# Kernel tuning notes

Measured on AMD Instinct MI355X. Metric: run time of the kernel, lower is better.

## Reference

```python
import jax, jax.numpy as jnp
import numpy as np

B, N, E, F, G = 32, 512, 4, 128, 64
EMB, HID = 128, 256  # NodeEmbedding: Linear(E*G=256 -> 256) + BN + ELU + Linear(256 -> 128)
NUM_EDGES = 8192
BN_EPS = 1e-5


def setup_inputs() -> dict:
    key = jax.random.key(0)
    ks = jax.random.split(key, 8)
    X = jax.random.normal(ks[0], (B, N, F), dtype=jnp.float32)
    edges = jax.random.randint(ks[1], (B, E, 2, NUM_EDGES), 0, N, dtype=jnp.int64)
    # per-edge-type projection W_e: [F, G] (glorot)
    Ws = jax.random.normal(ks[2], (E, F, G), dtype=jnp.float32) * np.sqrt(2.0 / (F + G))
    # attention vectors a_e: [2G, 1]
    a = jax.random.normal(ks[3], (E, 2 * G, 1), dtype=jnp.float32) * (1.414 * np.sqrt(2.0 / (2 * G + 1)))
    lin0_w = jax.random.normal(ks[4], (E * G, HID), dtype=jnp.float32) * np.sqrt(2.0 / (E * G + HID))
    lin0_b = jnp.zeros((HID,), dtype=jnp.float32)
    bn_gamma = jnp.ones((HID,), dtype=jnp.float32)
    bn_beta = jnp.zeros((HID,), dtype=jnp.float32)
    lin1_w = jax.random.normal(ks[5], (HID, EMB), dtype=jnp.float32) * np.sqrt(2.0 / (HID + EMB))
    lin1_b = jnp.zeros((EMB,), dtype=jnp.float32)
    return {"X": X, "edges": edges, "Ws": Ws, "a": a, "lin0_w": lin0_w,
            "lin0_b": lin0_b, "bn_gamma": bn_gamma, "bn_beta": bn_beta,
            "lin1_w": lin1_w, "lin1_b": lin1_b}


def _dense_adj(edges):
    # COO -> dense, summing duplicates like torch.sparse_coo_tensor(...).to_dense()
    b_ix = jnp.arange(B)[:, None, None]
    e_ix = jnp.arange(E)[None, :, None]
    src = edges[:, :, 0, :]
    dst = edges[:, :, 1, :]
    A = jnp.zeros((B, E, N, N), dtype=jnp.float32)
    return A.at[b_ix, e_ix, src, dst].add(1.0)


def reference(X, edges, Ws, a, lin0_w, lin0_b, bn_gamma, bn_beta, lin1_w, lin1_b):
    A = _dense_adj(edges)                                   # [B,E,N,N]
    Wh = jnp.einsum('bnf,efg->beng', X, Ws)                 # [B,E,N,G]
    Wh1 = jnp.einsum('beng,ego->beno', Wh, a[:, :G, :])     # [B,E,N,1]
    Wh2 = jnp.einsum('beng,ego->beno', Wh, a[:, G:, :])     # [B,E,N,1]
    scores = (Wh1 + jnp.swapaxes(Wh2, 2, 3)) * A            # [B,E,N,N] (masked-to-0, NOT -inf: faithful)
    att = jax.nn.softmax(scores, axis=-1)
    H = jnp.einsum('benm,bemg->beng', att * A, Wh)          # [B,E,N,G]
    H = jnp.transpose(H, (0, 2, 1, 3)).reshape(B * N, E * G)
    # NodeEmbedding MLP (BatchNorm1d in training mode: batch stats, biased var)
    h = H @ lin0_w + lin0_b
    mu = jnp.mean(h, axis=0)
    var = jnp.mean((h - mu) ** 2, axis=0)
    h = (h - mu) * jax.lax.rsqrt(var + BN_EPS) * bn_gamma + bn_beta
    h = jax.nn.elu(h)
    out = h @ lin1_w + lin1_b
    return out.reshape(B, N, EMB)
```

## Files before the change

### kernel.cpp

```cpp
#include <hip/hip_runtime.h>

#define Bx 32
#define Nx 512
#define Ex 4
#define Fx 128
#define Gx 64
#define HIDx 256
#define EMBx 128
#define NEDGE 8192

typedef __attribute__((ext_vector_type(8))) short bf16x8;
typedef __attribute__((ext_vector_type(4))) float f32x4;

#define L2E 1.44269504f

__device__ __forceinline__ ushort f2bf(float x) {
    unsigned int u = __float_as_uint(x);
    u += 0x7fffu + ((u >> 16) & 1u);
    return (ushort)(u >> 16);
}
__device__ __forceinline__ float bf2f(ushort h) {
    return __uint_as_float(((unsigned int)h) << 16);
}

__global__ __launch_bounds__(512) void k0b(const int* __restrict__ edges,
                                           const float* __restrict__ w0,
                                           const float* __restrict__ w1f,
                                           const float* __restrict__ Wsf,
                                           ushort* __restrict__ W0T,
                                           ushort* __restrict__ W1T,
                                           ushort* __restrict__ WsT,
                                           ushort* __restrict__ binned,
                                           int* __restrict__ offs) {
    __shared__ int hist8[8][8];
    __shared__ int offl[9];
    __shared__ int cur[8];
    int blk = blockIdx.x, tid = threadIdx.x;
    if (blk < 128) {
        int wave = tid >> 6;
        if (tid < 64) ((int*)hist8)[tid] = 0;
        __syncthreads();
        const int4* s4p = (const int4*)(edges + (size_t)blk * 2 * NEDGE);
        const int4* d4p = (const int4*)(edges + (size_t)blk * 2 * NEDGE + NEDGE);
        for (int i = tid; i < NEDGE / 4; i += 512) {
            int4 s4 = s4p[i];
            atomicAdd(&hist8[wave][s4.x >> 6], 1);
            atomicAdd(&hist8[wave][s4.y >> 6], 1);
            atomicAdd(&hist8[wave][s4.z >> 6], 1);
            atomicAdd(&hist8[wave][s4.w >> 6], 1);
        }
        __syncthreads();
        if (tid == 0) {
            int run = 0;
            for (int t = 0; t < 8; ++t) {
                offl[t] = run;
                int s = 0;
                #pragma unroll
                for (int w = 0; w < 8; ++w) s += hist8[w][t];
                run += s;
            }
            offl[8] = run;
            for (int t = 0; t <= 8; ++t) offs[blk * 9 + t] = offl[t];
        }
        __syncthreads();
        if (tid < 8) cur[tid] = offl[tid];
        __syncthreads();
        ushort* bout = binned + (size_t)blk * NEDGE;
        for (int i = tid; i < NEDGE / 4; i += 512) {
            int4 s4 = s4p[i]; int4 d4 = d4p[i];
            int ss[4] = {s4.x, s4.y, s4.z, s4.w};
            int dd[4] = {d4.x, d4.y, d4.z, d4.w};
            #pragma unroll
            for (int u = 0; u < 4; ++u) {
                int t = ss[u] >> 6;
                int pos = atomicAdd(&cur[t], 1);
                bout[pos] = (ushort)(((ss[u] & 63) << 9) | dd[u]);
            }
        }
    } else if (blk < 256) {
        int idx = (blk - 128) * 512 + tid;
        int j = idx >> 8, k = idx & 255;
        W0T[j * HIDx + k] = f2bf(w0[k * HIDx + j]);
    } else if (blk < 320) {
        int idx = (blk - 256) * 512 + tid;
        int j = idx >> 8, k = idx & 255;
        W1T[j * HIDx + k] = f2bf(w1f[k * EMBx + j]);
    } else {
        int idx = (blk - 320) * 512 + tid;
        int eg = idx >> 7, f = idx & 127;
        WsT[eg * Fx + f] = f2bf(Wsf[((eg >> 6) * Fx + f) * Gx + (eg & 63)]);
    }
}

__global__ __launch_bounds__(256) void k1_wh(const float* __restrict__ X,
                                             const ushort* __restrict__ WsT,
                                             const float* __restrict__ a,
                                             ushort* __restrict__ Whb,
                                             float* __restrict__ w1,
                                             float* __restrict__ w2) {
    __shared__ ushort sXb[64 * 128];
    int id = blockIdx.x;
    int e = id & 3;
    int rest = id >> 2;
    int tile = rest & 7;
    int b = rest >> 3;
    int be = b * 4 + e;
    int n0 = tile * 64;
    int tid = threadIdx.x;
    for (int i = tid; i < 2048; i += 256) {
        int row = i >> 5, kq = i & 31;
        float4 xv = *(const float4*)&X[(size_t)(b * Nx + n0 + row) * Fx + kq * 4];
        ushort4 hv;
        hv.x = f2bf(xv.x); hv.y = f2bf(xv.y); hv.z = f2bf(xv.z); hv.w = f2bf(xv.w);
        unsigned int byteo = ((unsigned int)(row * 256 + kq * 8)) ^ (((unsigned int)(row & 7)) << 4);
        *(ushort4*)((char*)sXb + byteo) = hv;
    }
    __syncthreads();
    int wave = tid >> 6, lane = tid & 63;
    int arow = lane & 15, kg = lane >> 4;
    int row = wave * 16 + arow;
    f32x4 acc[4];
    #pragma unroll
    for (int t = 0; t < 4; ++t) acc[t] = (f32x4){0.f, 0.f, 0.f, 0.f};
    const ushort* WT = WsT + e * Gx * Fx;
    unsigned int aswz = ((unsigned int)(row & 7)) << 4;
    #pragma unroll
    for (int ks = 0; ks < 4; ++ks) {
        unsigned int abyte = ((unsigned int)(row * 256 + ks * 64 + kg * 16)) ^ aswz;
        bf16x8 af = *(const bf16x8*)((const char*)sXb + abyte);
        #pragma unroll
        for (int jt = 0; jt < 4; ++jt) {
            bf16x8 bf = *(const bf16x8*)&WT[(size_t)(jt * 16 + arow) * Fx + ks * 32 + kg * 8];
            acc[jt] = __builtin_amdgcn_mfma_f32_16x16x32_bf16(af, bf, acc[jt], 0, 0, 0);
        }
    }
    float a1v[4], a2v[4];
    #pragma unroll
    for (int jt = 0; jt < 4; ++jt) {
        a1v[jt] = a[e * 2 * Gx + jt * 16 + arow];
        a2v[jt] = a[e * 2 * Gx + Gx + jt * 16 + arow];
    }
    int m0 = n0 + wave * 16 + kg * 4;
    #pragma unroll
    for (int jt = 0; jt < 4; ++jt) {
        int g = jt * 16 + arow;
        ushort4 v;
        v.x = f2bf(acc[jt][0]); v.y = f2bf(acc[jt][1]);
        v.z = f2bf(acc[jt][2]); v.w = f2bf(acc[jt][3]);
        *(ushort4*)&Whb[((size_t)be * Gx + g) * Nx + m0] = v;
    }
    #pragma unroll
    for (int reg = 0; reg < 4; ++reg) {
        float p1 = acc[0][reg] * a1v[0] + acc[1][reg] * a1v[1] + acc[2][reg] * a1v[2] + acc[3][reg] * a1v[3];
        float p2 = acc[0][reg] * a2v[0] + acc[1][reg] * a2v[1] + acc[2][reg] * a2v[2] + acc[3][reg] * a2v[3];
        #pragma unroll
        for (int off = 1; off < 16; off <<= 1) {
            p1 += __shfl_xor(p1, off, 64);
            p2 += __shfl_xor(p2, off, 64);
        }
        if (arow == 0) {
            w1[be * Nx + m0 + reg] = p1;
            w2[be * Nx + m0 + reg] = p2;
        }
    }
}

__global__ __launch_bounds__(512) void k2_att(const ushort* __restrict__ binned,
                                              const int* __restrict__ offs,
                                              const ushort* __restrict__ Whb,
                                              const float* __restrict__ w1g,
                                              const float* __restrict__ w2g,
                                              ushort* __restrict__ Hb) {
    __shared__ ushort P[64 * 512];
    __shared__ float sw2[512];
    __shared__ float sw1[64];
    __shared__ float sinv[64];
    __shared__ float rowsum[64];
    __shared__ ushort olist[4096];
    __shared__ int ocnt;
    unsigned int* cnt = (unsigned int*)P;
    int be = blockIdx.x; int b = be >> 2; int e = be & 3;
    int tile = blockIdx.y; int n0 = tile * 64;
    int tid = threadIdx.x;
    for (int i = tid; i < 64 * 132; i += 512) cnt[i] = 0u;
    {
        uint4 z = {0u, 0u, 0u, 0u};
        uint4* pu = (uint4*)((char*)P + 33792);
        for (int i = tid; i < 1984; i += 512) pu[i] = z;
    }
    sw2[tid] = w2g[be * Nx + tid] * L2E;
    if (tid < 64) {
        sw1[tid] = w1g[be * Nx + n0 + tid] * L2E;
        rowsum[tid] = 512.f;
    }
    if (tid == 0) ocnt = 0;
    __syncthreads();
    int t0 = offs[be * 9 + tile], t1 = offs[be * 9 + tile + 1];
    const ushort* bin = binned + (size_t)be * NEDGE;
    int lane = tid & 63;
    for (int i = t0 + tid; i < t1; i += 512) {
        unsigned int pk = bin[i];
        unsigned int sh = (pk & 3u) * 8;
        unsigned int old = atomicAdd(&cnt[(pk >> 9) * 132 + ((pk & 511u) >> 2)], 1u << sh);
        bool own = ((old >> sh) & 255u) == 0u;
        unsigned long long m = __ballot(own);
        if (m) {
            int leader = __ffsll((long long)m) - 1;
            int base = 0;
            if (lane == leader) base = atomicAdd(&ocnt, __popcll(m));
            base = __shfl(base, leader, 64);
            if (own) {
                int ix = base + __popcll(m & ((1ull << lane) - 1ull));
                if (ix < 4096) olist[ix] = (ushort)pk;
            }
        }
    }
    __syncthreads();
    int tot = ocnt; if (tot > 4096) tot = 4096;
    const unsigned char* cb = (const unsigned char*)cnt;
    ushort pbv[8]; int pkv[8];
    #pragma unroll
    for (int u = 0; u < 8; ++u) {
        int i = tid + u * 512;
        int pk = -1; ushort pb = 0;
        if (i < tot) {
            pk = (int)olist[i];
            int r = pk >> 9, d = pk & 511;
            float c = (float)cb[r * 528 + d];
            float ew = __builtin_exp2f(fminf((sw1[r] + sw2[d]) * c, 120.f));
            atomicAdd(&rowsum[r], ew - 1.f);
            pb = f2bf(ew * c);
        }
        pkv[u] = pk; pbv[u] = pb;
    }
    __syncthreads();
    {
        uint4 z = {0u, 0u, 0u, 0u};
        uint4* pu = (uint4*)P;
        for (int i = tid; i < 2112; i += 512) pu[i] = z;
    }
    __syncthreads();
    #pragma unroll
    for (int u = 0; u < 8; ++u) {
        if (pkv[u] >= 0) {
            int r = pkv[u] >> 9, d = pkv[u] & 511;
            unsigned int byteo = ((unsigned int)(r * 1024 + d * 2)) ^ (((unsigned int)(r & 7)) << 4);
            *(ushort*)((char*)P + byteo) = pbv[u];
        }
    }
    if (tid < 64) sinv[tid] = 1.f / rowsum[tid];
    int wave = tid >> 6;
    int wr2 = wave >> 2, wc = wave & 3;
    int rowa = wr2 * 32 + (lane & 15);
    int rowb = rowa + 16;
    int kgrp = lane >> 4;
    const ushort* WB = Whb + (size_t)be * Gx * Nx;
    int g0 = wc * 16 + (lane & 15);
    const ushort* Bp = WB + (size_t)g0 * Nx + kgrp * 8;
    bf16x8 bpre0 = *(const bf16x8*)(Bp + 0 * 32);
    bf16x8 bpre1 = *(const bf16x8*)(Bp + 1 * 32);
    bf16x8 bpre2 = *(const bf16x8*)(Bp + 2 * 32);
    bf16x8 bpre3 = *(const bf16x8*)(Bp + 3 * 32);
    __syncthreads();
    f32x4 acca = {0.f, 0.f, 0.f, 0.f};
    f32x4 accb = {0.f, 0.f, 0.f, 0.f};
    unsigned int aswza = ((unsigned int)(rowa & 7)) << 4;
    __builtin_amdgcn_s_setprio(1);
    #pragma unroll
    for (int ks = 0; ks < 16; ++ks) {
        bf16x8 bfv;
        if (ks == 0) bfv = bpre0;
        else if (ks == 1) bfv = bpre1;
        else if (ks == 2) bfv = bpre2;
        else if (ks == 3) bfv = bpre3;
        else bfv = *(const bf16x8*)(Bp + ks * 32);
        unsigned int ka = (unsigned int)(ks * 64 + kgrp * 16);
        unsigned int offa = ((unsigned int)(rowa * 1024) + ka) ^ aswza;
        unsigned int offb = ((unsigned int)(rowb * 1024) + ka) ^ aswza;
        bf16x8 afa = *(const bf16x8*)((const char*)P + offa);
        bf16x8 afb = *(const bf16x8*)((const char*)P + offb);
        acca = __builtin_amdgcn_mfma_f32_16x16x32_bf16(afa, bfv, acca, 0, 0, 0);
        accb = __builtin_amdgcn_mfma_f32_16x16x32_bf16(afb, bfv, accb, 0, 0, 0);
    }
    __builtin_amdgcn_s_setprio(0);
    #pragma unroll
    for (int reg = 0; reg < 4; ++reg) {
        int ra = n0 + wr2 * 32 + kgrp * 4 + reg;
        float iva = sinv[wr2 * 32 + kgrp * 4 + reg];
        float ivb = sinv[wr2 * 32 + 16 + kgrp * 4 + reg];
        Hb[((size_t)(b * Nx) + ra) * (Ex * Gx) + e * Gx + wc * 16 + (lane & 15)] =
            f2bf(acca[reg] * iva);
        Hb[((size_t)(b * Nx) + ra + 16) * (Ex * Gx) + e * Gx + wc * 16 + (lane & 15)] =
            f2bf(accb[reg] * ivb);
    }
}

__global__ __launch_bounds__(256) void k3_lin0(const ushort* __restrict__ Hb,
                                               const ushort* __restrict__ W0T,
                                               const float* __restrict__ lin0_b,
                                               ushort* __restrict__ h_pre,
                                               float* __restrict__ partials) {
    __shared__ float red_s[2][256], red_q[2][256];
    int tid = threadIdx.x, wave = tid >> 6, lane = tid & 63;
    int wr = wave >> 1, wc = wave & 1;
    int row0 = blockIdx.x * 32 + wr * 16;
    int arow = lane & 15, kg = lane >> 4;
    const ushort* A = Hb + (size_t)(row0 + arow) * HIDx;
    f32x4 acc[8];
    #pragma unroll
    for (int t = 0; t < 8; ++t) acc[t] = (f32x4){0.f, 0.f, 0.f, 0.f};
    #pragma unroll
    for (int ks = 0; ks < 8; ++ks) {
        int k0 = ks * 32 + kg * 8;
        bf16x8 af = *(const bf16x8*)&A[k0];
        #pragma unroll
        for (int jt = 0; jt < 8; ++jt) {
            bf16x8 bf = *(const bf16x8*)&W0T[(size_t)(wc * 128 + jt * 16 + arow) * HIDx + k0];
            acc[jt] = __builtin_amdgcn_mfma_f32_16x16x32_bf16(af, bf, acc[jt], 0, 0, 0);
        }
    }
    #pragma unroll
    for (int jt = 0; jt < 8; ++jt) {
        int col = wc * 128 + jt * 16 + arow;
        float b = lin0_b[col];
        float s = 0.f, q = 0.f;
        #pragma unroll
        for (int reg = 0; reg < 4; ++reg) {
            float v = acc[jt][reg] + b;
            h_pre[(size_t)(row0 + kg * 4 + reg) * HIDx + col] = f2bf(v);
            s += v; q += v * v;
        }
        s += __shfl_xor(s, 16, 64); s += __shfl_xor(s, 32, 64);
        q += __shfl_xor(q, 16, 64); q += __shfl_xor(q, 32, 64);
        if (lane < 16) { red_s[wr][col] = s; red_q[wr][col] = q; }
    }
    __syncthreads();
    int j = tid;
    partials[(size_t)blockIdx.x * 2 * HIDx + j] = red_s[0][j] + red_s[1][j];
    partials[(size_t)blockIdx.x * 2 * HIDx + HIDx + j] = red_q[0][j] + red_q[1][j];
}

__global__ __launch_bounds__(256) void k3b_stats(const float* __restrict__ partials,
                                                 const float* __restrict__ gamma,
                                                 const float* __restrict__ beta,
                                                 float* __restrict__ sb) {
    __shared__ float rs[8][32], rq[8][32];
    int jl = threadIdx.x & 31, sl = threadIdx.x >> 5;
    int j = blockIdx.x * 32 + jl;
    float s = 0.f, q = 0.f;
    for (int blk = sl; blk < 512; blk += 8) {
        s += partials[blk * 512 + j];
        q += partials[blk * 512 + 256 + j];
    }
    rs[sl][jl] = s; rq[sl][jl] = q;
    __syncthreads();
    if (threadIdx.x < 32) {
        float S = 0.f, Q = 0.f;
        #pragma unroll
        for (int t = 0; t < 8; ++t) { S += rs[t][jl]; Q += rq[t][jl]; }
        const float invM = 1.f / 16384.f;
        float mu = S * invM;
        float var = fmaxf(Q * invM - mu * mu, 0.f);
        float sc = gamma[j] * rsqrtf(var + 1e-5f);
        sb[j] = sc;
        sb[256 + j] = beta[j] - mu * sc;
    }
}

__global__ __launch_bounds__(256) void k4_lin1(const ushort* __restrict__ h_pre,
                                               const float* __restrict__ sb,
                                               const ushort* __restrict__ W1T,
                                               const float* __restrict__ lin1_b,
                                               float* __restrict__ out) {
    int tid = threadIdx.x, wave = tid >> 6, lane = tid & 63;
    int wr = wave >> 1, wc = wave & 1;
    int row0 = blockIdx.x * 32 + wr * 16;
    int arow = lane & 15, kg = lane >> 4;
    const ushort* A = h_pre + (size_t)(row0 + arow) * HIDx;
    f32x4 acc[4];
    #pragma unroll
    for (int t = 0; t < 4; ++t) acc[t] = (f32x4){0.f, 0.f, 0.f, 0.f};
    #pragma unroll
    for (int ks = 0; ks < 8; ++ks) {
        int k0 = ks * 32 + kg * 8;
        bf16x8 hv = *(const bf16x8*)&A[k0];
        float4 sc0 = *(const float4*)&sb[k0];
        float4 sc1 = *(const float4*)&sb[k0 + 4];
        float4 bi0 = *(const float4*)&sb[256 + k0];
        float4 bi1 = *(const float4*)&sb[256 + k0 + 4];
        float scv[8] = {sc0.x, sc0.y, sc0.z, sc0.w, sc1.x, sc1.y, sc1.z, sc1.w};
        float biv[8] = {bi0.x, bi0.y, bi0.z, bi0.w, bi1.x, bi1.y, bi1.z, bi1.w};
        bf16x8 af;
        #pragma unroll
        for (int u = 0; u < 8; ++u) {
            float v = bf2f((ushort)hv[u]) * scv[u] + biv[u];
            v = v > 0.f ? v : expm1f(v);
            af[u] = (short)f2bf(v);
        }
        #pragma unroll
        for (int jt = 0; jt < 4; ++jt) {
            bf16x8 bf = *(const bf16x8*)&W1T[(size_t)(wc * 64 + jt * 16 + arow) * HIDx + k0];
            acc[jt] = __builtin_amdgcn_mfma_f32_16x16x32_bf16(af, bf, acc[jt], 0, 0, 0);
        }
    }
    #pragma unroll
    for (int jt = 0; jt < 4; ++jt) {
        int col = wc * 64 + jt * 16 + arow;
        float b = lin1_b[col];
        #pragma unroll
        for (int reg = 0; reg < 4; ++reg)
            out[(size_t)(row0 + kg * 4 + reg) * EMBx + col] = acc[jt][reg] + b;
    }
}

extern "C" void kernel_launch(void* const* d_in, const int* in_sizes, int n_in,
                              void* d_out, int out_size, void* d_ws, size_t ws_size,
                              hipStream_t stream) {
    const float* X      = (const float*)d_in[0];
    const int*   edges  = (const int*)d_in[1];
    const float* Ws     = (const float*)d_in[2];
    const float* a      = (const float*)d_in[3];
    const float* lin0_w = (const float*)d_in[4];
    const float* lin0_b = (const float*)d_in[5];
    const float* gamma  = (const float*)d_in[6];
    const float* beta   = (const float*)d_in[7];
    const float* lin1_w = (const float*)d_in[8];
    const float* lin1_b = (const float*)d_in[9];
    float* ws = (float*)d_ws;

    ushort* Whb     = (ushort*)ws;
    ushort* h_pre   = (ushort*)ws;
    ushort* binned  = (ushort*)ws + 4194304;
    int*    offs    = (int*)(ws + 2621440);
    ushort* Hb      = (ushort*)(ws + 4194304);
    float*  w1      = ws + 8388608;
    float*  w2      = ws + 8454144;
    float*  partials= ws + 8519680;
    float*  sb      = ws + 8781824;
    ushort* WsT     = (ushort*)(ws + 8782336);
    ushort* W0T     = (ushort*)(ws + 8798720);
    ushort* W1T     = (ushort*)(ws + 8831488);
    float*  out     = (float*)d_out;

    k0b    <<<dim3(384), 512, 0, stream>>>(edges, lin0_w, lin1_w, Ws, W0T, W1T, WsT, binned, offs);
    k1_wh  <<<dim3(1024), 256, 0, stream>>>(X, WsT, a, Whb, w1, w2);
    k2_att <<<dim3(Bx * Ex, Nx / 64), 512, 0, stream>>>(binned, offs, Whb, w1, w2, Hb);
    k3_lin0<<<dim3(512), 256, 0, stream>>>(Hb, W0T, lin0_b, h_pre, partials);
    k3b_stats<<<8, 256, 0, stream>>>(partials, gamma, beta, sb);
    k4_lin1<<<dim3(512), 256, 0, stream>>>(h_pre, sb, W1T, lin1_b, out);
}
```

Baseline: 122.5 us.

## Fuse lin0, BN stats and lin1 into one cooperative kernel with LDS-resident activations

Merges the three MLP kernels into a single cooperative launch that uses grid-wide syncs between lin0+partial stats, BN stat reduction, and lin1. The pre-activation h tile stays in swizzled shared memory instead of being written to and re-read from global memory. This removes two kernel launches and the h_pre round trip through HBM. In exchange it pays for two grid barriers and requires all 512 blocks to be co-resident, and the extra 16KB of shared memory may limit occupancy.

```diff
diff --git a/kernel.cpp b/kernel.cpp
--- a/kernel.cpp
+++ b/kernel.cpp
@@ -1,4 +1,7 @@
 #include <hip/hip_runtime.h>
+#include <hip/hip_cooperative_groups.h>
+
+namespace cg = cooperative_groups;
 
 #define Bx 32
 #define Nx 512
@@ -295,121 +298,123 @@
     }
 }
 
-__global__ __launch_bounds__(256) void k3_lin0(const ushort* __restrict__ Hb,
-                                               const ushort* __restrict__ W0T,
-                                               const float* __restrict__ lin0_b,
-                                               ushort* __restrict__ h_pre,
-                                               float* __restrict__ partials) {
+__global__ __launch_bounds__(256) void k34(const ushort* __restrict__ Hb,
+                                           const ushort* __restrict__ W0T,
+                                           const float* __restrict__ lin0_b,
+                                           const float* __restrict__ gamma,
+                                           const float* __restrict__ beta,
+                                           const ushort* __restrict__ W1T,
+                                           const float* __restrict__ lin1_b,
+                                           float* __restrict__ partials,
+                                           float* __restrict__ sb,
+                                           float* __restrict__ out) {
+    __shared__ ushort sH[32 * 256];
     __shared__ float red_s[2][256], red_q[2][256];
+    cg::grid_group grid = cg::this_grid();
+    int bx = blockIdx.x;
     int tid = threadIdx.x, wave = tid >> 6, lane = tid & 63;
     int wr = wave >> 1, wc = wave & 1;
-    int row0 = blockIdx.x * 32 + wr * 16;
+    int row0 = bx * 32 + wr * 16;
     int arow = lane & 15, kg = lane >> 4;
-    const ushort* A = Hb + (size_t)(row0 + arow) * HIDx;
-    f32x4 acc[8];
-    #pragma unroll
-    for (int t = 0; t < 8; ++t) acc[t] = (f32x4){0.f, 0.f, 0.f, 0.f};
-    #pragma unroll
-    for (int ks = 0; ks < 8; ++ks) {
-        int k0 = ks * 32 + kg * 8;
-        bf16x8 af = *(const bf16x8*)&A[k0];
+    {
+        const ushort* A = Hb + (size_t)(row0 + arow) * HIDx;
+        f32x4 acc[8];
+        #pragma unroll
+        for (int t = 0; t < 8; ++t) acc[t] = (f32x4){0.f, 0.f, 0.f, 0.f};
+        #pragma unroll
+        for (int ks = 0; ks < 8; ++ks) {
+            int k0 = ks * 32 + kg * 8;
+            bf16x8 af = *(const bf16x8*)&A[k0];
+            #pragma unroll
+            for (int jt = 0; jt < 8; ++jt) {
+                bf16x8 bf = *(const bf16x8*)&W0T[(size_t)(wc * 128 + jt * 16 + arow) * HIDx + k0];
+                acc[jt] = __builtin_amdgcn_mfma_f32_16x16x32_bf16(af, bf, acc[jt], 0, 0, 0);
+            }
+        }
         #pragma unroll
         for (int jt = 0; jt < 8; ++jt) {
-            bf16x8 bf = *(const bf16x8*)&W0T[(size_t)(wc * 128 + jt * 16 + arow) * HIDx + k0];
-            acc[jt] = __builtin_amdgcn_mfma_f32_16x16x32_bf16(af, bf, acc[jt], 0, 0, 0);
-        }
-    }
-    #pragma unroll
-    for (int jt = 0; jt < 8; ++jt) {
-        int col = wc * 128 + jt * 16 + arow;
-        float b = lin0_b[col];
+            int col = wc * 128 + jt * 16 + arow;
+            float b = lin0_b[col];
+            float s = 0.f, q = 0.f;
+            #pragma unroll
+            for (int reg = 0; reg < 4; ++reg) {
+                float v = acc[jt][reg] + b;
+                int rl = wr * 16 + kg * 4 + reg;
+                unsigned int off = ((unsigned int)(rl * 512 + col * 2)) ^ (((unsigned int)(rl & 7)) << 4);
+                *(ushort*)((char*)sH + off) = f2bf(v);
+                s += v; q += v * v;
+            }
+            s += __shfl_xor(s, 16, 64); s += __shfl_xor(s, 32, 64);
+            q += __shfl_xor(q, 16, 64); q += __shfl_xor(q, 32, 64);
+            if (lane < 16) { red_s[wr][col] = s; red_q[wr][col] = q; }
+        }
+        __syncthreads();
+        partials[(size_t)bx * 2 * HIDx + tid] = red_s[0][tid] + red_s[1][tid];
+        partials[(size_t)bx * 2 * HIDx + HIDx + tid] = red_q[0][tid] + red_q[1][tid];
+    }
+    grid.sync();
+    if (bx < 64) {
+        int col = bx * 4 + (tid >> 6);
         float s = 0.f, q = 0.f;
         #pragma unroll
-        for (int reg = 0; reg < 4; ++reg) {
-            float v = acc[jt][reg] + b;
-            h_pre[(size_t)(row0 + kg * 4 + reg) * HIDx + col] = f2bf(v);
-            s += v; q += v * v;
-        }
-        s += __shfl_xor(s, 16, 64); s += __shfl_xor(s, 32, 64);
-        q += __shfl_xor(q, 16, 64); q += __shfl_xor(q, 32, 64);
-        if (lane < 16) { red_s[wr][col] = s; red_q[wr][col] = q; }
-    }
-    __syncthreads();
-    int j = tid;
-    partials[(size_t)blockIdx.x * 2 * HIDx + j] = red_s[0][j] + red_s[1][j];
-    partials[(size_t)blockIdx.x * 2 * HIDx + HIDx + j] = red_q[0][j] + red_q[1][j];
-}
-
-__global__ __launch_bounds__(256) void k3b_stats(const float* __restrict__ partials,
-                                                 const float* __restrict__ gamma,
-                                                 const float* __restrict__ beta,
-                                                 float* __restrict__ sb) {
-    __shared__ float rs[8][32], rq[8][32];
-    int jl = threadIdx.x & 31, sl = threadIdx.x >> 5;
-    int j = blockIdx.x * 32 + jl;
-    float s = 0.f, q = 0.f;
-    for (int blk = sl; blk < 512; blk += 8) {
-        s += partials[blk * 512 + j];
-        q += partials[blk * 512 + 256 + j];
-    }
-    rs[sl][jl] = s; rq[sl][jl] = q;
-    __syncthreads();
-    if (threadIdx.x < 32) {
-        float S = 0.f, Q = 0.f;
-        #pragma unroll
-        for (int t = 0; t < 8; ++t) { S += rs[t][jl]; Q += rq[t][jl]; }
-        const float invM = 1.f / 16384.f;
-        float mu = S * invM;
-        float var = fmaxf(Q * invM - mu * mu, 0.f);
-        float sc = gamma[j] * rsqrtf(var + 1e-5f);
-        sb[j] = sc;
-        sb[256 + j] = beta[j] - mu * sc;
-    }
-}
-
-__global__ __launch_bounds__(256) void k4_lin1(const ushort* __restrict__ h_pre,
-                                               const float* __restrict__ sb,
-                                               const ushort* __restrict__ W1T,
-                                               const float* __restrict__ lin1_b,
-                                               float* __restrict__ out) {
-    int tid = threadIdx.x, wave = tid >> 6, lane = tid & 63;
-    int wr = wave >> 1, wc = wave & 1;
-    int row0 = blockIdx.x * 32 + wr * 16;
-    int arow = lane & 15, kg = lane >> 4;
-    const ushort* A = h_pre + (size_t)(row0 + arow) * HIDx;
-    f32x4 acc[4];
-    #pragma unroll
-    for (int t = 0; t < 4; ++t) acc[t] = (f32x4){0.f, 0.f, 0.f, 0.f};
-    #pragma unroll
-    for (int ks = 0; ks < 8; ++ks) {
-        int k0 = ks * 32 + kg * 8;
-        bf16x8 hv = *(const bf16x8*)&A[k0];
-        float4 sc0 = *(const float4*)&sb[k0];
-        float4 sc1 = *(const float4*)&sb[k0 + 4];
-        float4 bi0 = *(const float4*)&sb[256 + k0];
-        float4 bi1 = *(const float4*)&sb[256 + k0 + 4];
-        float scv[8] = {sc0.x, sc0.y, sc0.z, sc0.w, sc1.x, sc1.y, sc1.z, sc1.w};
-        float biv[8] = {bi0.x, bi0.y, bi0.z, bi0.w, bi1.x, bi1.y, bi1.z, bi1.w};
-        bf16x8 af;
-        #pragma unroll
         for (int u = 0; u < 8; ++u) {
-            float v = bf2f((ushort)hv[u]) * scv[u] + biv[u];
-            v = v > 0.f ? v : expm1f(v);
-            af[u] = (short)f2bf(v);
+            int blk = lane * 8 + u;
+            s += partials[(size_t)blk * 512 + col];
+            q += partials[(size_t)blk * 512 + 256 + col];
+        }
+        #pragma unroll
+        for (int off = 1; off < 64; off <<= 1) {
+            s += __shfl_xor(s, off, 64);
+            q += __shfl_xor(q, off, 64);
+        }
+        if (lane == 0) {
+            const float invM = 1.f / 16384.f;
+            float mu = s * invM;
+            float var = fmaxf(q * invM - mu * mu, 0.f);
+            float sc = gamma[col] * rsqrtf(var + 1e-5f);
+            sb[col] = sc;
+            sb[256 + col] = beta[col] - mu * sc;
+        }
+    }
+    grid.sync();
+    {
+        f32x4 acc[4];
+        #pragma unroll
+        for (int t = 0; t < 4; ++t) acc[t] = (f32x4){0.f, 0.f, 0.f, 0.f};
+        int rl = wr * 16 + arow;
+        unsigned int rswz = ((unsigned int)(rl & 7)) << 4;
+        #pragma unroll
+        for (int ks = 0; ks < 8; ++ks) {
+            int k0 = ks * 32 + kg * 8;
+            unsigned int off = ((unsigned int)(rl * 512 + k0 * 2)) ^ rswz;
+            bf16x8 hv = *(const bf16x8*)((const char*)sH + off);
+            float4 sc0 = *(const float4*)&sb[k0];
+            float4 sc1 = *(const float4*)&sb[k0 + 4];
+            float4 bi0 = *(const float4*)&sb[256 + k0];
+            float4 bi1 = *(const float4*)&sb[256 + k0 + 4];
+            float scv[8] = {sc0.x, sc0.y, sc0.z, sc0.w, sc1.x, sc1.y, sc1.z, sc1.w};
+            float biv[8] = {bi0.x, bi0.y, bi0.z, bi0.w, bi1.x, bi1.y, bi1.z, bi1.w};
+            bf16x8 af;
+            #pragma unroll
+            for (int u = 0; u < 8; ++u) {
+                float v = bf2f((ushort)hv[u]) * scv[u] + biv[u];
+                v = v > 0.f ? v : expm1f(v);
+                af[u] = (short)f2bf(v);
+            }
+            #pragma unroll
+            for (int jt = 0; jt < 4; ++jt) {
+                bf16x8 bf = *(const bf16x8*)&W1T[(size_t)(wc * 64 + jt * 16 + arow) * HIDx + k0];
+                acc[jt] = __builtin_amdgcn_mfma_f32_16x16x32_bf16(af, bf, acc[jt], 0, 0, 0);
+            }
         }
         #pragma unroll
         for (int jt = 0; jt < 4; ++jt) {
-            bf16x8 bf = *(const bf16x8*)&W1T[(size_t)(wc * 64 + jt * 16 + arow) * HIDx + k0];
-            acc[jt] = __builtin_amdgcn_mfma_f32_16x16x32_bf16(af, bf, acc[jt], 0, 0, 0);
-        }
-    }
-    #pragma unroll
-    for (int jt = 0; jt < 4; ++jt) {
-        int col = wc * 64 + jt * 16 + arow;
-        float b = lin1_b[col];
-        #pragma unroll
-        for (int reg = 0; reg < 4; ++reg)
-            out[(size_t)(row0 + kg * 4 + reg) * EMBx + col] = acc[jt][reg] + b;
+            int col = wc * 64 + jt * 16 + arow;
+            float b = lin1_b[col];
+            #pragma unroll
+            for (int reg = 0; reg < 4; ++reg)
+                out[(size_t)(row0 + kg * 4 + reg) * EMBx + col] = acc[jt][reg] + b;
+        }
     }
 }
 
@@ -429,7 +434,6 @@
     float* ws = (float*)d_ws;
 
     ushort* Whb     = (ushort*)ws;
-    ushort* h_pre   = (ushort*)ws;
     ushort* binned  = (ushort*)ws + 4194304;
     int*    offs    = (int*)(ws + 2621440);
     ushort* Hb      = (ushort*)(ws + 4194304);
@@ -445,7 +449,10 @@
     k0b    <<<dim3(384), 512, 0, stream>>>(edges, lin0_w, lin1_w, Ws, W0T, W1T, WsT, binned, offs);
     k1_wh  <<<dim3(1024), 256, 0, stream>>>(X, WsT, a, Whb, w1, w2);
     k2_att <<<dim3(Bx * Ex, Nx / 64), 512, 0, stream>>>(binned, offs, Whb, w1, w2, Hb);
-    k3_lin0<<<dim3(512), 256, 0, stream>>>(Hb, W0T, lin0_b, h_pre, partials);
-    k3b_stats<<<8, 256, 0, stream>>>(partials, gamma, beta, sb);
-    k4_lin1<<<dim3(512), 256, 0, stream>>>(h_pre, sb, W1T, lin1_b, out);
-}
+
+    const ushort* Hb_c = Hb; const ushort* W0T_c = W0T; const ushort* W1T_c = W1T;
+    void* args[] = {(void*)&Hb_c, (void*)&W0T_c, (void*)&lin0_b, (void*)&gamma,
+                    (void*)&beta, (void*)&W1T_c, (void*)&lin1_b,
+                    (void*)&partials, (void*)&sb, (void*)&out};
+    hipLaunchCooperativeKernel((const void*)k34, dim3(512), dim3(256), args, 0, stream);
+}
```

Result: slower. 207.1 us (+69.1%).
